# Kernel optimization log

Measured on AMD Instinct MI355X. Metric: run time of the kernel, lower is better.

The kernel has to match this reference:

```python
import jax, jax.numpy as jnp
import numpy as np

B, S, D, H = 64, 64, 4096, 64  # NOTE: code requires S == H (see notes)
HD = D // H  # 64


def setup_inputs() -> dict:
    key = jax.random.key(0)
    ks = jax.random.split(key, 9)
    std = 0.02
    return {
        "x": jax.random.normal(ks[0], (B, S, D), dtype=jnp.float32),
        "Wq": jax.random.normal(ks[1], (D, D), dtype=jnp.float32) * std,
        "bq": jax.random.normal(ks[2], (D,), dtype=jnp.float32) * std,
        "Wk": jax.random.normal(ks[3], (D, D), dtype=jnp.float32) * std,
        "bk": jax.random.normal(ks[4], (D,), dtype=jnp.float32) * std,
        "Wv": jax.random.normal(ks[5], (D, D), dtype=jnp.float32) * std,
        "bv": jax.random.normal(ks[6], (D,), dtype=jnp.float32) * std,
        "Wp": jax.random.normal(ks[7], (D, D), dtype=jnp.float32) * std,
        "bp": jax.random.normal(ks[8], (D,), dtype=jnp.float32) * std,
    }


def reference(x, Wq, bq, Wk, bk, Wv, bv, Wp, bp):
    b, s, d = x.shape
    h, hd = H, d // H
    # q, k: [B,S,D] -> [B,S,H,hd] -> [B,H,S,hd]
    q = (x @ Wq.T + bq).reshape(b, s, h, hd).transpose(0, 2, 1, 3)
    k = (x @ Wk.T + bk).reshape(b, s, h, hd).transpose(0, 2, 1, 3)
    # v: faithfully replicates the original buggy view(B, H, S, hd).transpose(1,2)
    # -> shape [B, S, H, hd] (NOT head-major)
    v = (x @ Wv.T + bv).reshape(b, h, s, hd).transpose(0, 2, 1, 3)
    # attention WITHOUT 1/sqrt(hd) scaling (faithful to source)
    attn = jax.nn.softmax(jnp.einsum("bhqd,bhkd->bhqk", q, k), axis=-1)  # [B,H,S,S]
    # dropout layers are identity in eval mode
    # ShardedTensor: chunk v along last dim into 2 shards of hd/2
    v0, v1 = jnp.split(v, 2, axis=-1)  # each [B,S,H,hd/2]; broadcast needs S==H
    out0 = jnp.matmul(attn, v0)  # [B,H,S,hd/2]
    out1 = jnp.matmul(attn, v1)
    out = jnp.concatenate([out0, out1], axis=0)  # [2B,H,S,hd/2] (faithful cat on dim 0)
    out = out.transpose(0, 2, 1, 3).reshape(b, s, d)  # row-major regroup, same as torch view
    return out @ Wp.T + bp
```

## Files before the change

### kernel.cpp

```cpp
#include <hip/hip_runtime.h>
#include <stdint.h>

typedef __bf16   bf16x8  __attribute__((ext_vector_type(8)));
typedef float    f32x4   __attribute__((ext_vector_type(4)));
typedef uint16_t u16x8   __attribute__((ext_vector_type(8)));

using as1_cvp = const __attribute__((address_space(1))) void*;
using as3_vp  = __attribute__((address_space(3))) void*;

__device__ __forceinline__ uint16_t f2bf(float f) {
    uint32_t u = __float_as_uint(f);
    u += 0x7FFF + ((u >> 16) & 1);
    return (uint16_t)(u >> 16);
}

__device__ __forceinline__ void gload16(const void* g, void* l) {
    __builtin_amdgcn_global_load_lds((as1_cvp)g, (as3_vp)l, 16, 0, 0);
}

#define MFMA16(a, b, c) __builtin_amdgcn_mfma_f32_16x16x32_bf16((a), (b), (c), 0, 0, 0)

__global__ __launch_bounds__(256)
void cvt_bf16(const float* __restrict__ in, uint16_t* __restrict__ out, int n8)
{
    int i = blockIdx.x * 256 + threadIdx.x;
    if (i >= n8) return;
    const float4* p = reinterpret_cast<const float4*>(in) + (size_t)i * 2;
    float4 a = p[0], b = p[1];
    u16x8 o;
    o[0] = f2bf(a.x); o[1] = f2bf(a.y); o[2] = f2bf(a.z); o[3] = f2bf(a.w);
    o[4] = f2bf(b.x); o[5] = f2bf(b.y); o[6] = f2bf(b.z); o[7] = f2bf(b.w);
    reinterpret_cast<u16x8*>(out)[i] = o;
}

template <int OUT_BF16>
__global__ __launch_bounds__(512, 2)
void gemm256(const uint16_t* __restrict__ A, const uint16_t* __restrict__ Bt,
             const float* __restrict__ bias, void* __restrict__ Cout,
             int M, int N, int K)
{
    __shared__ uint16_t lds[65536];
    const int NT = K >> 6;

    int bid = blockIdx.x;
    bid = (bid & 7) * 32 + (bid >> 3);
    const int bx = bid & 15, by = bid >> 4;
    const int rb = by * 256, cb = bx * 256;

    const int tid  = threadIdx.x;
    const int w    = tid >> 6;
    const int lane = tid & 63;
    const int g    = lane >> 4;
    const int l16  = lane & 15;
    const int wm   = w >> 2;
    const int wn   = w & 3;
    const int srow = lane >> 2;
    const int sblk = lane & 3;

    f32x4 acc[8][4] = {};

    auto stageA = [&](int buf, int kh, int kbase) {
#pragma unroll
        for (int i = 0; i < 2; ++i) {
            const int row = i * 128 + w * 16 + srow;
            const uint16_t* src = A + (size_t)(rb + row) * K + kbase
                                    + ((sblk ^ ((row >> 1) & 3)) << 3);
            gload16(src, &lds[(buf * 2 + kh) * 16384 + i * 4096 + w * 512]);
        }
    };
    auto stageB = [&](int buf, int kh, int kbase) {
#pragma unroll
        for (int i = 0; i < 2; ++i) {
            const int row = i * 128 + w * 16 + srow;
            const uint16_t* src = Bt + (size_t)(cb + row) * K + kbase
                                     + ((sblk ^ ((row >> 1) & 3)) << 3);
            gload16(src, &lds[(buf * 2 + kh) * 16384 + 8192 + i * 4096 + w * 512]);
        }
    };

    auto readA = [&](int base, int grp, bf16x8* dst) {
#pragma unroll
        for (int mi = 0; mi < 4; ++mi) {
            const int r = wm * 128 + grp * 64 + mi * 16 + l16;
            dst[mi] = *reinterpret_cast<const bf16x8*>(
                &lds[base + r * 32 + ((g ^ ((r >> 1) & 3)) << 3)]);
        }
    };
    auto readB = [&](int base, bf16x8* dst) {
#pragma unroll
        for (int n = 0; n < 4; ++n) {
            const int c = wn * 64 + n * 16 + l16;
            dst[n] = *reinterpret_cast<const bf16x8*>(
                &lds[base + 8192 + c * 32 + ((g ^ ((c >> 1) & 3)) << 3)]);
        }
    };

    auto mfma_grp = [&](int grp, const bf16x8* af, const bf16x8* bf) {
        __builtin_amdgcn_s_setprio(1);
#pragma unroll
        for (int mi = 0; mi < 4; ++mi)
#pragma unroll
            for (int n = 0; n < 4; ++n)
                acc[grp * 4 + mi][n] = MFMA16(af[mi], bf[n], acc[grp * 4 + mi][n]);
        __builtin_amdgcn_s_setprio(0);
    };

    stageA(0, 0, 0);  stageB(0, 0, 0);
    stageA(0, 1, 32); stageB(0, 1, 32);
    stageA(1, 0, 64); stageB(1, 0, 64);
    asm volatile("s_waitcnt vmcnt(4)" ::: "memory");
    __builtin_amdgcn_s_barrier();

    for (int t = 0; t < NT; ++t) {
        const int cur = t & 1, nxt = cur ^ 1;
        const int b0 = (cur * 2 + 0) * 16384;
        const int b1 = (cur * 2 + 1) * 16384;
        bf16x8 af0[4], af1[4], af2[4], af3[4], bf0[4], bf1[4];

        if (t + 1 < NT) stageA(nxt, 1, (t + 1) * 64 + 32);
        readA(b0, 0, af0); readB(b0, bf0);
        readA(b0, 1, af1);
        mfma_grp(0, af0, bf0);
        __builtin_amdgcn_sched_barrier(0);
        __builtin_amdgcn_s_barrier();

        if (t + 1 < NT) stageB(nxt, 1, (t + 1) * 64 + 32);
        readB(b1, bf1);
        readA(b1, 0, af2);
        mfma_grp(1, af1, bf0);
        __builtin_amdgcn_sched_barrier(0);
        __builtin_amdgcn_s_barrier();

        if (t + 2 < NT) stageA(cur, 0, (t + 2) * 64);
        readA(b1, 1, af3);
        mfma_grp(0, af2, bf1);
        __builtin_amdgcn_sched_barrier(0);
        __builtin_amdgcn_s_barrier();

        if (t + 2 < NT) stageB(cur, 0, (t + 2) * 64);
        mfma_grp(1, af3, bf1);
        __builtin_amdgcn_sched_barrier(0);
        if (t >= NT - 2) asm volatile("s_waitcnt vmcnt(0)" ::: "memory");
        else             asm volatile("s_waitcnt vmcnt(4)" ::: "memory");
        __builtin_amdgcn_s_barrier();
    }

    float bv[4];
#pragma unroll
    for (int n = 0; n < 4; ++n) bv[n] = bias[cb + wn * 64 + n * 16 + l16];

#pragma unroll
    for (int m = 0; m < 8; ++m) {
#pragma unroll
        for (int n = 0; n < 4; ++n) {
            const int col = cb + wn * 64 + n * 16 + l16;
#pragma unroll
            for (int r = 0; r < 4; ++r) {
                const int row = rb + wm * 128 + m * 16 + g * 4 + r;
                float v = acc[m][n][r] + bv[n];
                if (OUT_BF16)
                    ((uint16_t*)Cout)[(size_t)row * N + col] = f2bf(v);
                else
                    ((float*)Cout)[(size_t)row * N + col] = v;
            }
        }
    }
}

__global__ __launch_bounds__(256)
void attn_kernel(const uint16_t* __restrict__ Q, const uint16_t* __restrict__ Kg,
                 const uint16_t* __restrict__ V, uint16_t* __restrict__ Y)
{
    const int bid = blockIdx.x;
    const int hh  = bid & 63;
    const int bb  = bid >> 6;
    const int tid = threadIdx.x;
    const int w   = tid >> 6, lane = tid & 63, g = lane >> 4, l16 = lane & 15;

    __shared__ uint16_t Vt[64 * 64];
    __shared__ uint16_t Pl[64 * 64];

    {
        const int k  = tid >> 2;
        const int l0 = (tid & 3) * 16;
        const uint16_t* src = V + (size_t)(bb * 64 + k) * 4096 + hh * 64 + l0;
        u16x8 v0 = *reinterpret_cast<const u16x8*>(src);
        u16x8 v1 = *reinterpret_cast<const u16x8*>(src + 8);
#pragma unroll
        for (int i = 0; i < 8; ++i) {
            int l = l0 + i;
            Vt[l * 64 + (k ^ ((l & 7) << 3))] = v0[i];
        }
#pragma unroll
        for (int i = 0; i < 8; ++i) {
            int l = l0 + 8 + i;
            Vt[l * 64 + (k ^ ((l & 7) << 3))] = v1[i];
        }
    }

    f32x4 sa[4] = {};
    {
        const uint16_t* qrow = Q + (size_t)(bb * 64 + w * 16 + l16) * 4096 + hh * 64 + g * 8;
        bf16x8 a0 = *reinterpret_cast<const bf16x8*>(qrow);
        bf16x8 a1 = *reinterpret_cast<const bf16x8*>(qrow + 32);
#pragma unroll
        for (int n = 0; n < 4; ++n) {
            const uint16_t* krow = Kg + (size_t)(bb * 64 + n * 16 + l16) * 4096 + hh * 64 + g * 8;
            bf16x8 b0 = *reinterpret_cast<const bf16x8*>(krow);
            bf16x8 b1 = *reinterpret_cast<const bf16x8*>(krow + 32);
            sa[n] = MFMA16(a0, b0, sa[n]);
            sa[n] = MFMA16(a1, b1, sa[n]);
        }
    }

    float p[4][4];
#pragma unroll
    for (int j = 0; j < 4; ++j) {
        float mx = fmaxf(fmaxf(sa[0][j], sa[1][j]), fmaxf(sa[2][j], sa[3][j]));
        mx = fmaxf(mx, __shfl_xor(mx, 1));
        mx = fmaxf(mx, __shfl_xor(mx, 2));
        mx = fmaxf(mx, __shfl_xor(mx, 4));
        mx = fmaxf(mx, __shfl_xor(mx, 8));
        float s = 0.f;
#pragma unroll
        for (int n = 0; n < 4; ++n) { p[n][j] = __expf(sa[n][j] - mx); s += p[n][j]; }
        s += __shfl_xor(s, 1);
        s += __shfl_xor(s, 2);
        s += __shfl_xor(s, 4);
        s += __shfl_xor(s, 8);
        float inv = 1.0f / s;
#pragma unroll
        for (int n = 0; n < 4; ++n) p[n][j] *= inv;
    }

#pragma unroll
    for (int j = 0; j < 4; ++j) {
        const int q = w * 16 + g * 4 + j;
#pragma unroll
        for (int n = 0; n < 4; ++n) {
            const int kcol = n * 16 + l16;
            Pl[q * 64 + (kcol ^ ((q & 7) << 3))] = f2bf(p[n][j]);
        }
    }
    __syncthreads();

    f32x4 oa[4] = {};
    {
        const int qr = w * 16 + l16;
        bf16x8 a0 = *reinterpret_cast<const bf16x8*>(&Pl[qr * 64 + ((g * 8)      ^ ((qr & 7) << 3))]);
        bf16x8 a1 = *reinterpret_cast<const bf16x8*>(&Pl[qr * 64 + ((32 + g * 8) ^ ((qr & 7) << 3))]);
#pragma unroll
        for (int n = 0; n < 4; ++n) {
            const int vr = n * 16 + l16;
            bf16x8 b0 = *reinterpret_cast<const bf16x8*>(&Vt[vr * 64 + ((g * 8)      ^ ((vr & 7) << 3))]);
            bf16x8 b1 = *reinterpret_cast<const bf16x8*>(&Vt[vr * 64 + ((32 + g * 8) ^ ((vr & 7) << 3))]);
            oa[n] = MFMA16(a0, b0, oa[n]);
            oa[n] = MFMA16(a1, b1, oa[n]);
        }
    }

#pragma unroll
    for (int n = 0; n < 4; ++n) {
        const int ll = n * 16 + l16;
#pragma unroll
        for (int r = 0; r < 4; ++r) {
            const int qq = w * 16 + g * 4 + r;
            const int b_ = (bb >> 1) + ((ll >= 32) ? 32 : 0);
            const int s_ = ((bb & 1) << 5) + (qq >> 1);
            const int h_ = ((qq & 1) << 5) + (hh >> 1);
            const int l_ = ((hh & 1) << 5) + (ll & 31);
            Y[(size_t)(b_ * 64 + s_) * 4096 + h_ * 64 + l_] = f2bf(oa[n][r]);
        }
    }
}

extern "C" void kernel_launch(void* const* d_in, const int* in_sizes, int n_in,
                              void* d_out, int out_size, void* d_ws, size_t ws_size,
                              hipStream_t stream)
{
    (void)in_sizes; (void)n_in; (void)out_size; (void)ws_size;

    const float* x  = (const float*)d_in[0];
    const float* Wq = (const float*)d_in[1];
    const float* bq = (const float*)d_in[2];
    const float* Wk = (const float*)d_in[3];
    const float* bk = (const float*)d_in[4];
    const float* Wv = (const float*)d_in[5];
    const float* bv = (const float*)d_in[6];
    const float* Wp = (const float*)d_in[7];
    const float* bp = (const float*)d_in[8];
    float* out = (float*)d_out;

    const size_t NN = 16777216;
    uint16_t* xb   = (uint16_t*)d_ws;
    uint16_t* wb   = xb + NN;
    uint16_t* Qb   = wb + NN;
    uint16_t* Kb   = Qb + NN;
    uint16_t* Vb   = Kb + NN;
    uint16_t* Yb   = xb;

    const int n8 = (int)(NN / 8);
    dim3 cgrid((n8 + 255) / 256), cblk(256);
    dim3 ggrid(256), gblk(512);

    cvt_bf16<<<cgrid, cblk, 0, stream>>>(x, xb, n8);

    cvt_bf16<<<cgrid, cblk, 0, stream>>>(Wq, wb, n8);
    gemm256<1><<<ggrid, gblk, 0, stream>>>(xb, wb, bq, (void*)Qb, 4096, 4096, 4096);

    cvt_bf16<<<cgrid, cblk, 0, stream>>>(Wk, wb, n8);
    gemm256<1><<<ggrid, gblk, 0, stream>>>(xb, wb, bk, (void*)Kb, 4096, 4096, 4096);

    cvt_bf16<<<cgrid, cblk, 0, stream>>>(Wv, wb, n8);
    gemm256<1><<<ggrid, gblk, 0, stream>>>(xb, wb, bv, (void*)Vb, 4096, 4096, 4096);

    attn_kernel<<<dim3(4096), dim3(256), 0, stream>>>(Qb, Kb, Vb, Yb);

    cvt_bf16<<<cgrid, cblk, 0, stream>>>(Wp, wb, n8);
    gemm256<0><<<ggrid, gblk, 0, stream>>>(Yb, wb, bp, (void*)out, 4096, 4096, 4096);
}
```

Before: 598.9 us.

## Fuse fp32-to-bf16 weight conversion into GEMM B-operand staging

Drops the four separate weight conversion kernels and has each GEMM load fp32 weights straight into registers, convert them to bf16 and write them into LDS, with the prefetch pipeline and waitcnts reworked around the register path. This removes a full read and write pass over each 64 MB weight matrix plus four launches. In exchange every GEMM tile reads twice as many bytes for B, since fp32 weights are re-read by each row-block, and loses the asynchronous global-to-LDS path for B, adding register pressure and VALU conversion work inside the main loop.

```diff
diff --git a/kernel.cpp b/kernel.cpp
--- a/kernel.cpp
+++ b/kernel.cpp
@@ -35,7 +35,7 @@
 
 template <int OUT_BF16>
 __global__ __launch_bounds__(512, 2)
-void gemm256(const uint16_t* __restrict__ A, const uint16_t* __restrict__ Bt,
+void gemm256(const uint16_t* __restrict__ A, const float* __restrict__ Bt,
              const float* __restrict__ bias, void* __restrict__ Cout,
              int M, int N, int K)
 {
@@ -68,13 +68,25 @@
             gload16(src, &lds[(buf * 2 + kh) * 16384 + i * 4096 + w * 512]);
         }
     };
-    auto stageB = [&](int buf, int kh, int kbase) {
+    auto loadB = [&](int kbase, float4* dst) {
 #pragma unroll
         for (int i = 0; i < 2; ++i) {
             const int row = i * 128 + w * 16 + srow;
-            const uint16_t* src = Bt + (size_t)(cb + row) * K + kbase
-                                     + ((sblk ^ ((row >> 1) & 3)) << 3);
-            gload16(src, &lds[(buf * 2 + kh) * 16384 + 8192 + i * 4096 + w * 512]);
+            const float* s = Bt + (size_t)(cb + row) * K + kbase
+                               + ((sblk ^ ((row >> 1) & 3)) << 3);
+            dst[i * 2 + 0] = *reinterpret_cast<const float4*>(s);
+            dst[i * 2 + 1] = *reinterpret_cast<const float4*>(s + 4);
+        }
+    };
+    auto writeB = [&](int buf, int kh, const float4* src) {
+#pragma unroll
+        for (int i = 0; i < 2; ++i) {
+            const float4 lo = src[i * 2], hi = src[i * 2 + 1];
+            u16x8 o;
+            o[0] = f2bf(lo.x); o[1] = f2bf(lo.y); o[2] = f2bf(lo.z); o[3] = f2bf(lo.w);
+            o[4] = f2bf(hi.x); o[5] = f2bf(hi.y); o[6] = f2bf(hi.z); o[7] = f2bf(hi.w);
+            *reinterpret_cast<u16x8*>(
+                &lds[(buf * 2 + kh) * 16384 + 8192 + i * 4096 + w * 512 + lane * 8]) = o;
         }
     };
 
@@ -105,10 +117,14 @@
         __builtin_amdgcn_s_setprio(0);
     };
 
-    stageA(0, 0, 0);  stageB(0, 0, 0);
-    stageA(0, 1, 32); stageB(0, 1, 32);
-    stageA(1, 0, 64); stageB(1, 0, 64);
-    asm volatile("s_waitcnt vmcnt(4)" ::: "memory");
+    float4 q0[4], q1[4], pb0[4];
+    stageA(0, 0, 0);   loadB(0,  q0);
+    stageA(0, 1, 32);  loadB(32, q1);
+    stageA(1, 0, 64);  loadB(64, pb0);
+    asm volatile("s_waitcnt vmcnt(6)" ::: "memory");
+    writeB(0, 0, q0);
+    writeB(0, 1, q1);
+    asm volatile("s_waitcnt lgkmcnt(0)" ::: "memory");
     __builtin_amdgcn_s_barrier();
 
     for (int t = 0; t < NT; ++t) {
@@ -116,6 +132,7 @@
         const int b0 = (cur * 2 + 0) * 16384;
         const int b1 = (cur * 2 + 1) * 16384;
         bf16x8 af0[4], af1[4], af2[4], af3[4], bf0[4], bf1[4];
+        float4 pb1[4];
 
         if (t + 1 < NT) stageA(nxt, 1, (t + 1) * 64 + 32);
         readA(b0, 0, af0); readB(b0, bf0);
@@ -124,11 +141,18 @@
         __builtin_amdgcn_sched_barrier(0);
         __builtin_amdgcn_s_barrier();
 
-        if (t + 1 < NT) stageB(nxt, 1, (t + 1) * 64 + 32);
+        if (t + 1 < NT) loadB((t + 1) * 64 + 32, pb1);
+        mfma_grp(1, af1, bf0);
+        __builtin_amdgcn_sched_barrier(0);
+        if (t + 1 < NT) {
+            if (t + 2 < NT) asm volatile("s_waitcnt vmcnt(6)" ::: "memory");
+            else            asm volatile("s_waitcnt vmcnt(0)" ::: "memory");
+            writeB(nxt, 0, pb0);
+        }
+        __builtin_amdgcn_sched_barrier(0);
         readB(b1, bf1);
         readA(b1, 0, af2);
-        mfma_grp(1, af1, bf0);
-        __builtin_amdgcn_sched_barrier(0);
+        asm volatile("s_waitcnt lgkmcnt(8)" ::: "memory");
         __builtin_amdgcn_s_barrier();
 
         if (t + 2 < NT) stageA(cur, 0, (t + 2) * 64);
@@ -137,11 +161,15 @@
         __builtin_amdgcn_sched_barrier(0);
         __builtin_amdgcn_s_barrier();
 
-        if (t + 2 < NT) stageB(cur, 0, (t + 2) * 64);
+        if (t + 2 < NT) loadB((t + 2) * 64, pb0);
         mfma_grp(1, af3, bf1);
         __builtin_amdgcn_sched_barrier(0);
-        if (t >= NT - 2) asm volatile("s_waitcnt vmcnt(0)" ::: "memory");
-        else             asm volatile("s_waitcnt vmcnt(4)" ::: "memory");
+        if (t + 1 < NT) {
+            if (t + 2 < NT) asm volatile("s_waitcnt vmcnt(6)" ::: "memory");
+            else            asm volatile("s_waitcnt vmcnt(0)" ::: "memory");
+            writeB(nxt, 1, pb1);
+            asm volatile("s_waitcnt lgkmcnt(0)" ::: "memory");
+        }
         __builtin_amdgcn_s_barrier();
     }
 
@@ -293,8 +321,7 @@
 
     const size_t NN = 16777216;
     uint16_t* xb   = (uint16_t*)d_ws;
-    uint16_t* wb   = xb + NN;
-    uint16_t* Qb   = wb + NN;
+    uint16_t* Qb   = xb + NN;
     uint16_t* Kb   = Qb + NN;
     uint16_t* Vb   = Kb + NN;
     uint16_t* Yb   = xb;
@@ -305,17 +332,11 @@
 
     cvt_bf16<<<cgrid, cblk, 0, stream>>>(x, xb, n8);
 
-    cvt_bf16<<<cgrid, cblk, 0, stream>>>(Wq, wb, n8);
-    gemm256<1><<<ggrid, gblk, 0, stream>>>(xb, wb, bq, (void*)Qb, 4096, 4096, 4096);
-
-    cvt_bf16<<<cgrid, cblk, 0, stream>>>(Wk, wb, n8);
-    gemm256<1><<<ggrid, gblk, 0, stream>>>(xb, wb, bk, (void*)Kb, 4096, 4096, 4096);
-
-    cvt_bf16<<<cgrid, cblk, 0, stream>>>(Wv, wb, n8);
-    gemm256<1><<<ggrid, gblk, 0, stream>>>(xb, wb, bv, (void*)Vb, 4096, 4096, 4096);
+    gemm256<1><<<ggrid, gblk, 0, stream>>>(xb, Wq, bq, (void*)Qb, 4096, 4096, 4096);
+    gemm256<1><<<ggrid, gblk, 0, stream>>>(xb, Wk, bk, (void*)Kb, 4096, 4096, 4096);
+    gemm256<1><<<ggrid, gblk, 0, stream>>>(xb, Wv, bv, (void*)Vb, 4096, 4096, 4096);
 
     attn_kernel<<<dim3(4096), dim3(256), 0, stream>>>(Qb, Kb, Vb, Yb);
 
-    cvt_bf16<<<cgrid, cblk, 0, stream>>>(Wp, wb, n8);
-    gemm256<0><<<ggrid, gblk, 0, stream>>>(Yb, wb, bp, (void*)out, 4096, 4096, 4096);
-}
+    gemm256<0><<<ggrid, gblk, 0, stream>>>(Yb, Wp, bp, (void*)out, 4096, 4096, 4096);
+}
```

Result: slower. 820.4 us (+37.0%).
